# Kernel tuning notes

Measured on AMD Instinct MI355X. Metric: run time of the kernel, lower is better.

## Reference

```python
import jax, jax.numpy as jnp
import numpy as np

B, T, N, H, NHEADS, DFF, DEMO = 128, 128, 76, 64, 4, 256, 12

def _lin(x, W, b):
    # torch Linear: y = x @ W.T + b, W is [out, in]
    return jnp.matmul(x, W.T) + b

def _layernorm(x, g, b, eps=1e-7):
    mu = x.mean(-1, keepdims=True)
    var = ((x - mu) ** 2).mean(-1, keepdims=True)
    return (x - mu) / jnp.sqrt(var + eps) * g + b

def _gru_all_features(X, Wih, Whh, bih, bhh):
    # X: [B,T,N]; Wih: [N,3H] (input_size=1); Whh: [N,3H,H]; biases [N,3H]
    # PyTorch gate order: r, z, n. Returns H_seq [B,N,T,H].
    Bsz, Tlen, Nf = X.shape
    Hd = Whh.shape[-1]
    h0 = jnp.zeros((Bsz, Nf, Hd), X.dtype)
    def step(h, x_t):  # h [B,N,H], x_t [B,N]
        ih = x_t[:, :, None] * Wih[None] + bih[None]            # [B,N,3H]
        hh = jnp.einsum('bnh,ngh->bng', h, Whh) + bhh[None]     # [B,N,3H]
        r = jax.nn.sigmoid(ih[..., :Hd] + hh[..., :Hd])
        z = jax.nn.sigmoid(ih[..., Hd:2 * Hd] + hh[..., Hd:2 * Hd])
        n = jnp.tanh(ih[..., 2 * Hd:] + r * hh[..., 2 * Hd:])
        h_new = (1.0 - z) * n + z * h
        return h_new, h_new
    _, Hs = jax.lax.scan(step, h0, jnp.moveaxis(X, 1, 0))       # [T,B,N,H]
    return jnp.transpose(Hs, (1, 2, 0, 3))                      # [B,N,T,H]

def _time_attention(Hs, Wt, bt, Wx, bx, rate):
    # Hs [B,N,T,H]; Wt/Wx [N,H,H]; bt/bx [N,H]; rate [N]
    Tlen = Hs.shape[2]
    q = jnp.einsum('bnh,nkh->bnk', Hs[:, :, -1, :], Wt) + bt[None]          # [B,N,H]
    K = jnp.einsum('bnth,nkh->bntk', Hs, Wx) + bx[None, :, None, :]         # [B,N,T,H]
    dot = jnp.einsum('bnk,bntk->bnt', q, K)                                 # [B,N,T]
    tdecay = jnp.arange(1, Tlen + 1, dtype=Hs.dtype)                        # [1..T]
    ds = jax.nn.sigmoid(dot)
    denom = jax.nn.sigmoid(rate)[None, :, None] * jnp.log(2.72 + (1.0 - ds)) * tdecay
    denom = jnp.maximum(denom, 1e-6)
    e = jax.nn.relu(ds / denom)
    alpha = jax.nn.softmax(e, axis=-1)
    return jnp.einsum('bnt,bnth->bnh', alpha, Hs)                           # [B,N,H]

def _mha_decov(x, Wq, bq, Wk, bk, Wv, bv, Wo, bo, n_heads):
    Bsz, L, Dm = x.shape
    dk = Dm // n_heads
    def split(t):
        return t.reshape(Bsz, L, n_heads, dk).transpose(0, 2, 1, 3)
    q, k, v = split(_lin(x, Wq, bq)), split(_lin(x, Wk, bk)), split(_lin(x, Wv, bv))
    scores = jnp.matmul(q, k.transpose(0, 1, 3, 2)) / (dk ** 0.5)
    attn = jax.nn.softmax(scores, axis=-1)
    head = jnp.matmul(attn, v)                                              # [B,h,L,dk]
    merged = head.transpose(0, 2, 1, 3).reshape(Bsz, L, Dm)
    out = _lin(merged, Wo, bo)
    U = merged.reshape(Bsz * L, Dm)
    U = U - U.mean(0, keepdims=True)
    C = (U.T @ U) / max(Bsz * L, 1)
    decov = 0.5 * ((C ** 2).sum() - (jnp.diag(C) ** 2).sum())
    return out, decov

def setup_inputs():
    key = jax.random.key(0)
    ks = jax.random.split(key, 32)
    s = 0.08
    def rn(k, shape):
        return jax.random.normal(k, shape, jnp.float32) * s
    inp = {
        'X': jax.random.normal(ks[0], (B, T, N), jnp.float32),
        'D': jax.random.normal(ks[1], (B, DEMO), jnp.float32),
        'gru_Wih': rn(ks[2], (N, 3 * H)),
        'gru_Whh': rn(ks[3], (N, 3 * H, H)),
        'gru_bih': jnp.zeros((N, 3 * H), jnp.float32),
        'gru_bhh': jnp.zeros((N, 3 * H), jnp.float32),
        'att_Wt': rn(ks[4], (N, H, H)),
        'att_bt': jnp.zeros((N, H), jnp.float32),
        'att_Wx': rn(ks[5], (N, H, H)),
        'att_bx': jnp.zeros((N, H), jnp.float32),
        'att_rate': jnp.zeros((N,), jnp.float32),
        'demo_W': rn(ks[6], (H, DEMO)),
        'demo_b': jnp.zeros((H,), jnp.float32),
        'mh_Wq': rn(ks[7], (H, H)), 'mh_bq': rn(ks[8], (H,)),
        'mh_Wk': rn(ks[9], (H, H)), 'mh_bk': rn(ks[10], (H,)),
        'mh_Wv': rn(ks[11], (H, H)), 'mh_bv': rn(ks[12], (H,)),
        'mh_Wo': rn(ks[13], (H, H)), 'mh_bo': rn(ks[14], (H,)),
        'ln1_g': jnp.ones((H,), jnp.float32), 'ln1_b': jnp.zeros((H,), jnp.float32),
        'ffn_W1': rn(ks[15], (DFF, H)), 'ffn_b1': rn(ks[16], (DFF,)),
        'ffn_W2': rn(ks[17], (H, DFF)), 'ffn_b2': rn(ks[18], (H,)),
        'ln2_g': jnp.ones((H,), jnp.float32), 'ln2_b': jnp.zeros((H,), jnp.float32),
        'fa_Wq': rn(ks[19], (H, H)), 'fa_bq': rn(ks[20], (H,)),
        'fa_Wk': rn(ks[21], (H, H)), 'fa_bk': rn(ks[22], (H,)),
        'fa_Wv': rn(ks[23], (H, H)), 'fa_bv': rn(ks[24], (H,)),
        'fa_Wout': rn(ks[25], (1, H)), 'fa_bout': rn(ks[26], (1,)),
        'out0_W': rn(ks[27], (H, H)), 'out0_b': jnp.zeros((H,), jnp.float32),
        'out1_W': rn(ks[28], (1, H)), 'out1_b': jnp.zeros((1,), jnp.float32),
    }
    return inp

def _forward(X, D, gru_Wih, gru_Whh, gru_bih, gru_bhh, att_Wt, att_bt, att_Wx, att_bx,
             att_rate, demo_W, demo_b, mh_Wq, mh_bq, mh_Wk, mh_bk, mh_Wv, mh_bv, mh_Wo,
             mh_bo, ln1_g, ln1_b, ffn_W1, ffn_b1, ffn_W2, ffn_b2, ln2_g, ln2_b,
             fa_Wq, fa_bq, fa_Wk, fa_bk, fa_Wv, fa_bv, fa_Wout, fa_bout,
             out0_W, out0_b, out1_W, out1_b):
    Hs = _gru_all_features(X, gru_Wih, gru_Whh, gru_bih, gru_bhh)   # [B,N,T,H]
    F_dyn = _time_attention(Hs, att_Wt, att_bt, att_Wx, att_bx, att_rate)  # [B,N,H]
    f_demo = jnp.tanh(_lin(D, demo_W, demo_b))[:, None, :]
    F_in = jnp.concatenate([F_dyn, f_demo], axis=1)                 # [B,N+1,H]
    _, decov = _mha_decov(F_in, mh_Wq, mh_bq, mh_Wk, mh_bk, mh_Wv, mh_bv, mh_Wo, mh_bo, NHEADS)
    attn_out, _ = _mha_decov(_layernorm(F_in, ln1_g, ln1_b), mh_Wq, mh_bq, mh_Wk, mh_bk,
                             mh_Wv, mh_bv, mh_Wo, mh_bo, NHEADS)
    Y = F_in + attn_out
    z = _layernorm(Y, ln2_g, ln2_b)
    Z = Y + _lin(jax.nn.relu(_lin(z, ffn_W1, ffn_b1)), ffn_W2, ffn_b2)
    # FinalAttentionQKV
    Q = _lin(Z, fa_Wq, fa_bq)
    K = _lin(Z, fa_Wk, fa_bk)
    V = _lin(Z, fa_Wv, fa_bv)
    scores = _lin(Q * K, fa_Wout, fa_bout)[..., 0]                  # [B,L]
    alpha = jax.nn.softmax(scores, axis=1)
    s = jnp.einsum('bl,blh->bh', alpha, V)
    h = jax.nn.relu(_lin(s, out0_W, out0_b))
    y_prob = jax.nn.sigmoid(_lin(h, out1_W, out1_b))
    return y_prob, decov

def reference(X, D, gru_Wih, gru_Whh, gru_bih, gru_bhh, att_Wt, att_bt, att_Wx, att_bx,
              att_rate, demo_W, demo_b, mh_Wq, mh_bq, mh_Wk, mh_bk, mh_Wv, mh_bv, mh_Wo,
              mh_bo, ln1_g, ln1_b, ffn_W1, ffn_b1, ffn_W2, ffn_b2, ln2_g, ln2_b,
              fa_Wq, fa_bq, fa_Wk, fa_bk, fa_Wv, fa_bv, fa_Wout, fa_bout,
              out0_W, out0_b, out1_W, out1_b):
    return _forward(X, D, gru_Wih, gru_Whh, gru_bih, gru_bhh, att_Wt, att_bt, att_Wx,
                    att_bx, att_rate, demo_W, demo_b, mh_Wq, mh_bq, mh_Wk, mh_bk, mh_Wv,
                    mh_bv, mh_Wo, mh_bo, ln1_g, ln1_b, ffn_W1, ffn_b1, ffn_W2, ffn_b2,
                    ln2_g, ln2_b, fa_Wq, fa_bq, fa_Wk, fa_bk, fa_Wv, fa_bv, fa_Wout,
                    fa_bout, out0_W, out0_b, out1_W, out1_b)
```

## Files before the change

kernel.cpp:

```cpp
#include <hip/hip_runtime.h>
#include <math.h>

#define B_ 128
#define T_ 128
#define NF 76
#define HD 64
#define LQ 77

typedef __attribute__((ext_vector_type(8))) short short8v;
typedef __attribute__((ext_vector_type(4))) short short4v;
typedef __attribute__((ext_vector_type(4))) float f32x4;

__device__ __forceinline__ float frcp(float x) { return __builtin_amdgcn_rcpf(x); }
__device__ __forceinline__ float sigmf(float x) { return frcp(1.0f + __expf(-x)); }
__device__ __forceinline__ float sigm2(float x) { return frcp(1.0f + __builtin_amdgcn_exp2f(-x)); }
__device__ __forceinline__ float tanh_fast(float x) { return 2.0f * frcp(1.0f + __expf(-2.0f * x)) - 1.0f; }
__device__ __forceinline__ short tobf(float x) {
    unsigned u = __float_as_uint(x);
    u += 0x7FFF + ((u >> 16) & 1);
    return (short)(u >> 16);
}
__device__ __forceinline__ float bflo(unsigned u) { return __uint_as_float(u << 16); }
__device__ __forceinline__ float bfhi(unsigned u) { return __uint_as_float(u & 0xffff0000u); }

__global__ __launch_bounds__(256) void k_gru0(
    const float* __restrict__ X, const float* __restrict__ Wih,
    const float* __restrict__ Whh, const float* __restrict__ bih,
    const float* __restrict__ bhh,
    const float* __restrict__ Wt, const float* __restrict__ bt,
    const float* __restrict__ Wx, const float* __restrict__ bx,
    short* __restrict__ Hsg, float* __restrict__ qxg, float* __restrict__ qbg)
{
    __shared__ short As[8][16 * 68];
    __shared__ float xs[16 * 129];
    __shared__ float q1[16 * 65];
    __shared__ float q2[16 * 65];

    const int nf = blockIdx.y;
    const int chunk = blockIdx.x;
    const int cbase = chunk * 16;
    const int tid = threadIdx.x;
    const int w = tid >> 6;
    const int lane = tid & 63;
    const int col = lane & 15;
    const int quad = lane >> 4;

    const float S1 = 1.44269504f;
    const float S2 = 2.88539008f;

    for (int i = tid; i < 16 * T_; i += 256) {
        int b = i >> 7, t = i & 127;
        xs[b * 129 + t] = X[((size_t)(cbase + b) * T_ + t) * NF + nf];
    }

    short8v bfr[3][2];
    const float* wbase = Whh + (size_t)nf * 12288;
#pragma unroll
    for (int g3 = 0; g3 < 3; ++g3) {
        const float sc = (g3 == 2) ? S2 : S1;
#pragma unroll
        for (int k2 = 0; k2 < 2; ++k2) {
            int g = 64 * g3 + 16 * w + col;
            const float* src = wbase + g * 64 + 32 * k2 + quad * 8;
            float4 f0 = *(const float4*)src;
            float4 f1 = *(const float4*)(src + 4);
            short8v fr;
            fr[0] = tobf(f0.x * sc); fr[1] = tobf(f0.y * sc);
            fr[2] = tobf(f0.z * sc); fr[3] = tobf(f0.w * sc);
            fr[4] = tobf(f1.x * sc); fr[5] = tobf(f1.y * sc);
            fr[6] = tobf(f1.z * sc); fr[7] = tobf(f1.w * sc);
            bfr[g3][k2] = fr;
        }
    }

    const int c = 16 * w + col;
    const int base = nf * 192;
    const float wr = Wih[base + c] * S1;
    const float wz = Wih[base + 64 + c] * S1;
    const float wn = Wih[base + 128 + c] * S2;
    const float br = (bih[base + c] + bhh[base + c]) * S1;
    const float bz = (bih[base + 64 + c] + bhh[base + 64 + c]) * S1;
    const float bnn = bih[base + 128 + c] * S2;
    const float bhn = bhh[base + 128 + c] * S2;

    for (int i = tid; i < 16 * 68; i += 256) As[7][i] = 0;
    float hold[4];
#pragma unroll
    for (int r = 0; r < 4; ++r) hold[r] = 0.0f;
    __syncthreads();

    for (int t = 0; t < T_; ++t) {
        const int rb = (t + 7) & 7;
        const int wb = t & 7;
        const short* ap = &As[rb][col * 68 + quad * 8];
        short4v a0 = *(const short4v*)ap;
        short4v a1 = *(const short4v*)(ap + 4);
        short4v a2 = *(const short4v*)(ap + 32);
        short4v a3 = *(const short4v*)(ap + 36);
        short8v A0 = {a0[0], a0[1], a0[2], a0[3], a1[0], a1[1], a1[2], a1[3]};
        short8v A1 = {a2[0], a2[1], a2[2], a2[3], a3[0], a3[1], a3[2], a3[3]};

        f32x4 acc[3];
#pragma unroll
        for (int g3 = 0; g3 < 3; ++g3) {
            f32x4 a = {0.0f, 0.0f, 0.0f, 0.0f};
            a = __builtin_amdgcn_mfma_f32_16x16x32_bf16(A0, bfr[g3][0], a, 0, 0, 0);
            a = __builtin_amdgcn_mfma_f32_16x16x32_bf16(A1, bfr[g3][1], a, 0, 0, 0);
            acc[g3] = a;
        }

#pragma unroll
        for (int r = 0; r < 4; ++r) {
            float xv = xs[(quad * 4 + r) * 129 + t];
            float rr = sigm2(xv * wr + br + acc[0][r]);
            float zz = sigm2(xv * wz + bz + acc[1][r]);
            float nn = 2.0f * sigm2(xv * wn + bnn + rr * (acc[2][r] + bhn)) - 1.0f;
            hold[r] = nn + zz * (hold[r] - nn);
        }

#pragma unroll
        for (int r = 0; r < 4; ++r)
            As[wb][(quad * 4 + r) * 68 + c] = tobf(hold[r]);
        __syncthreads();

        if ((t & 7) == 7) {
            const int oct = tid & 7, bb = (tid >> 3) & 15, k0 = tid >> 7;
            short4v r0[4], r1[4];
#pragma unroll
            for (int s = 0; s < 4; ++s) {
                const short* p = &As[k0 + 2 * s][bb * 68 + oct * 8];
                r0[s] = *(const short4v*)p;
                r1[s] = *(const short4v*)(p + 4);
            }
            __syncthreads();
            const size_t gbase =
                (((size_t)nf * 128 + cbase + bb) * 128 + (t - 7)) * 64 + oct * 8;
#pragma unroll
            for (int s = 0; s < 4; ++s) {
                short8v v = {r0[s][0], r0[s][1], r0[s][2], r0[s][3],
                             r1[s][0], r1[s][1], r1[s][2], r1[s][3]};
                *(short8v*)(Hsg + gbase + (size_t)(k0 + 2 * s) * 64) = v;
            }
        }
    }

#pragma unroll
    for (int r = 0; r < 4; ++r)
        q1[(quad * 4 + r) * 65 + c] = hold[r];
    __syncthreads();
    for (int o = tid; o < 16 * 64; o += 256) {
        int b = o >> 6, k = o & 63;
        const float* wrow = Wt + ((size_t)nf * 64 + k) * 64;
        float a = bt[nf * 64 + k];
#pragma unroll 8
        for (int h = 0; h < 64; h += 4) {
            float4 wv = *(const float4*)&wrow[h];
            a += q1[b * 65 + h] * wv.x + q1[b * 65 + h + 1] * wv.y
               + q1[b * 65 + h + 2] * wv.z + q1[b * 65 + h + 3] * wv.w;
        }
        q2[b * 65 + k] = a;
    }
    __syncthreads();
    for (int o = tid; o < 16 * 64; o += 256) {
        int b = o >> 6, h = o & 63;
        float a = 0.0f;
#pragma unroll 8
        for (int k = 0; k < 64; ++k)
            a += q2[b * 65 + k] * Wx[((size_t)nf * 64 + k) * 64 + h];
        qxg[((size_t)nf * 128 + cbase + b) * 64 + h] = a;
    }
    for (int b = tid; b < 16; b += 256) {
        float a = 0.0f;
        for (int k = 0; k < 64; ++k) a += q2[b * 65 + k] * bx[nf * 64 + k];
        qbg[nf * 128 + cbase + b] = a;
    }
}

__global__ __launch_bounds__(128) void k_att(
    const short* __restrict__ Hsg, const float* __restrict__ qxg,
    const float* __restrict__ qbg, const float* __restrict__ rate,
    const float* __restrict__ D, const float* __restrict__ dW,
    const float* __restrict__ db, float* __restrict__ Sz,
    float* __restrict__ Fin)
{
    const int nf = blockIdx.x, b = blockIdx.y;
    const int tid = threadIdx.x;

    if (nf == NF) {
        if (tid < 64) {
            float acc = db[tid];
            for (int j = 0; j < 12; ++j) acc += D[b * 12 + j] * dW[tid * 12 + j];
            Fin[((size_t)b * LQ + 76) * HD + tid] = tanh_fast(acc);
        }
        int s0 = b * 33;
        for (int k = tid; k < 33; k += 128) {
            int idx = s0 + k;
            if (idx < 4161) Sz[idx] = 0.0f;
        }
        return;
    }

    __shared__ float wsum[128 * 69];
    __shared__ float wl[128];
    __shared__ float qxl[64];
    __shared__ float pn[2][68];
    __shared__ float pd[2];
    if (tid < 64) qxl[tid] = qxg[((size_t)nf * 128 + b) * 64 + tid];
    const float qb = qbg[nf * 128 + b];
    const float sigr = sigmf(rate[nf]);

    uint4 rv[8];
    const uint4* src = (const uint4*)(Hsg + (((size_t)nf * 128 + b) * 128 + tid) * 64);
#pragma unroll
    for (int k = 0; k < 8; ++k) rv[k] = src[k];
    __syncthreads();

    float a = qb;
#pragma unroll
    for (int k = 0; k < 8; ++k) {
        a += bflo(rv[k].x) * qxl[k * 8 + 0] + bfhi(rv[k].x) * qxl[k * 8 + 1]
           + bflo(rv[k].y) * qxl[k * 8 + 2] + bfhi(rv[k].y) * qxl[k * 8 + 3]
           + bflo(rv[k].z) * qxl[k * 8 + 4] + bfhi(rv[k].z) * qxl[k * 8 + 5]
           + bflo(rv[k].w) * qxl[k * 8 + 6] + bfhi(rv[k].w) * qxl[k * 8 + 7];
    }
    float ds = sigmf(a);
    float dn = fmaxf(sigr * __logf(2.72f + (1.0f - ds)) * (float)(tid + 1), 1e-6f);
    float e = fmaxf(ds * frcp(dn), 0.0f);
    float w = __expf(e);
    wl[tid] = w;
#pragma unroll
    for (int k = 0; k < 8; ++k) {
        float* d = &wsum[tid * 69 + k * 8];
        d[0] = w * bflo(rv[k].x); d[1] = w * bfhi(rv[k].x);
        d[2] = w * bflo(rv[k].y); d[3] = w * bfhi(rv[k].y);
        d[4] = w * bflo(rv[k].z); d[5] = w * bfhi(rv[k].z);
        d[6] = w * bflo(rv[k].w); d[7] = w * bfhi(rv[k].w);
    }
    __syncthreads();
    {
        int ch = tid & 63, half = tid >> 6;
        float acc = 0.0f, den = 0.0f;
        int t0 = half * 64;
        for (int t = t0; t < t0 + 64; ++t) {
            acc += wsum[t * 69 + ch];
            den += wl[t];
        }
        pn[half][ch] = acc;
        if (ch == 0) pd[half] = den;
    }
    __syncthreads();
    if (tid < 64) {
        float num = pn[0][tid] + pn[1][tid];
        float den = pd[0] + pd[1];
        Fin[((size_t)b * LQ + nf) * HD + tid] = num * frcp(den);
    }
}

__global__ __launch_bounds__(256) void k_mha2(
    const float* __restrict__ Fin,
    const float* __restrict__ Wq, const float* __restrict__ bq,
    const float* __restrict__ Wk, const float* __restrict__ bk,
    const float* __restrict__ Wv, const float* __restrict__ bv,
    const float* __restrict__ g1, const float* __restrict__ b1,
    float* __restrict__ M1, float* __restrict__ M2)
{
    __shared__ float xl[LQ * 68];
    __shared__ float qh[LQ * 20], kh[LQ * 20], vh[LQ * 20];
    float (*os)[17] = (float (*)[17])xl;
    const int b = blockIdx.x, hd = blockIdx.y, v = blockIdx.z;
    const int tid = threadIdx.x;
    const float* xsrc = Fin + (size_t)b * LQ * HD;

    for (int idx = tid; idx < LQ * HD; idx += 256)
        xl[(idx >> 6) * 68 + (idx & 63)] = xsrc[idx];
    __syncthreads();
    if (v == 1) {
        if (tid < LQ) {
            float mu = 0.0f;
            for (int h = 0; h < 64; ++h) mu += xl[tid * 68 + h];
            mu *= (1.0f / 64.0f);
            float var = 0.0f;
            for (int h = 0; h < 64; ++h) { float d = xl[tid * 68 + h] - mu; var += d * d; }
            var *= (1.0f / 64.0f);
            float rs = rsqrtf(var + 1e-7f);
            for (int h = 0; h < 64; ++h)
                xl[tid * 68 + h] = (xl[tid * 68 + h] - mu) * rs * g1[h] + b1[h];
        }
        __syncthreads();
    }

    for (int idx = tid; idx < LQ * 16; idx += 256) {
        int l = idx >> 4, d = idx & 15, ch = hd * 16 + d;
        float aq = bq[ch], ak = bk[ch], av = bv[ch];
        const float4* wq = (const float4*)(Wq + ch * 64);
        const float4* wk = (const float4*)(Wk + ch * 64);
        const float4* wv = (const float4*)(Wv + ch * 64);
        const float4* xr = (const float4*)&xl[l * 68];
#pragma unroll 4
        for (int c4 = 0; c4 < 16; ++c4) {
            float4 xv = xr[c4];
            float4 a = wq[c4], bb = wk[c4], cc = wv[c4];
            aq += xv.x * a.x + xv.y * a.y + xv.z * a.z + xv.w * a.w;
            ak += xv.x * bb.x + xv.y * bb.y + xv.z * bb.z + xv.w * bb.w;
            av += xv.x * cc.x + xv.y * cc.y + xv.z * cc.z + xv.w * cc.w;
        }
        qh[l * 20 + d] = aq; kh[l * 20 + d] = ak; vh[l * 20 + d] = av;
    }
    __syncthreads();

    if (tid < 231) {
        int l = tid % 77, third = tid / 77;
        float4 qf0 = *(const float4*)&qh[l * 20 + 0];
        float4 qf1 = *(const float4*)&qh[l * 20 + 4];
        float4 qf2 = *(const float4*)&qh[l * 20 + 8];
        float4 qf3 = *(const float4*)&qh[l * 20 + 12];
        int j0 = third * 26;
        int j1 = (third == 2) ? LQ : j0 + 26;
        float o[16];
#pragma unroll
        for (int d = 0; d < 16; ++d) o[d] = 0.0f;
        float ss = 0.0f;
        for (int j = j0; j < j1; ++j) {
            const float4* kp = (const float4*)&kh[j * 20];
            float4 k0 = kp[0], k1 = kp[1], k2 = kp[2], k3 = kp[3];
            float sc = qf0.x * k0.x + qf0.y * k0.y + qf0.z * k0.z + qf0.w * k0.w
                     + qf1.x * k1.x + qf1.y * k1.y + qf1.z * k1.z + qf1.w * k1.w
                     + qf2.x * k2.x + qf2.y * k2.y + qf2.z * k2.z + qf2.w * k2.w
                     + qf3.x * k3.x + qf3.y * k3.y + qf3.z * k3.z + qf3.w * k3.w;
            float p = __expf(sc * 0.25f);
            ss += p;
            const float4* vp = (const float4*)&vh[j * 20];
            float4 v0 = vp[0], v1 = vp[1], v2 = vp[2], v3 = vp[3];
            o[0] += p * v0.x; o[1] += p * v0.y; o[2] += p * v0.z; o[3] += p * v0.w;
            o[4] += p * v1.x; o[5] += p * v1.y; o[6] += p * v1.z; o[7] += p * v1.w;
            o[8] += p * v2.x; o[9] += p * v2.y; o[10] += p * v2.z; o[11] += p * v2.w;
            o[12] += p * v3.x; o[13] += p * v3.y; o[14] += p * v3.z; o[15] += p * v3.w;
        }
#pragma unroll
        for (int d = 0; d < 16; ++d) os[tid][d] = o[d];
        os[tid][16] = ss;
    }
    __syncthreads();
    if (tid < LQ) {
        float inv = frcp(os[tid][16] + os[77 + tid][16] + os[154 + tid][16]);
        float* Mout = (v == 1) ? M2 : M1;
#pragma unroll
        for (int d = 0; d < 16; ++d)
            Mout[((size_t)b * LQ + tid) * HD + hd * 16 + d]
                = (os[tid][d] + os[77 + tid][d] + os[154 + tid][d]) * inv;
    }
}

__global__ __launch_bounds__(256) void k_zff(
    const float* __restrict__ Fin, float* __restrict__ M2,
    const float* __restrict__ Wo, const float* __restrict__ bo,
    const float* __restrict__ g2, const float* __restrict__ b2,
    const float* __restrict__ W1, const float* __restrict__ bb1,
    const float* __restrict__ W2, const float* __restrict__ bb2,
    const float* __restrict__ faWq, const float* __restrict__ fabq,
    const float* __restrict__ faWk, const float* __restrict__ fabk,
    const float* __restrict__ faWv, const float* __restrict__ fabv,
    const float* __restrict__ faWout, const float* __restrict__ fabout,
    float* __restrict__ scout)
{
    __shared__ float m2l[16 * 68];
    __shared__ float yl[16 * 68];
    __shared__ float zl[16 * 68];
    __shared__ float ul[16 * 260];
    const int tid = threadIdx.x;
    const size_t base = (size_t)blockIdx.x * 16;
    const size_t eb = base * 64;
    const int h = tid & 63, rq = tid >> 6;

    for (int idx = tid; idx < 1024; idx += 256)
        m2l[(idx >> 6) * 68 + (idx & 63)] = M2[eb + idx];
    __syncthreads();

    {
        float acc[4];
#pragma unroll
        for (int rr = 0; rr < 4; ++rr) acc[rr] = bo[h];
        const float4* wo = (const float4*)(Wo + h * 64);
#pragma unroll 4
        for (int c4 = 0; c4 < 16; ++c4) {
            float4 wv = wo[c4];
#pragma unroll
            for (int rr = 0; rr < 4; ++rr) {
                float4 mv = *(const float4*)&m2l[(rq * 4 + rr) * 68 + c4 * 4];
                acc[rr] += mv.x * wv.x + mv.y * wv.y + mv.z * wv.z + mv.w * wv.w;
            }
        }
#pragma unroll
        for (int rr = 0; rr < 4; ++rr) {
            int r = rq * 4 + rr;
            yl[r * 68 + h] = Fin[eb + r * 64 + h] + acc[rr];
        }
    }
    __syncthreads();
    if (tid < 16) {
        float mu = 0.0f;
        for (int c = 0; c < 64; ++c) mu += yl[tid * 68 + c];
        mu *= (1.0f / 64.0f);
        float var = 0.0f;
        for (int c = 0; c < 64; ++c) { float d = yl[tid * 68 + c] - mu; var += d * d; }
        var *= (1.0f / 64.0f);
        float rs = rsqrtf(var + 1e-7f);
        for (int c = 0; c < 64; ++c)
            zl[tid * 68 + c] = (yl[tid * 68 + c] - mu) * rs * g2[c] + b2[c];
    }
    __syncthreads();

    {
        const int f = tid;
        float acc[16];
#pragma unroll
        for (int r = 0; r < 16; ++r) acc[r] = bb1[f];
        const float4* w1r = (const float4*)(W1 + f * 64);
#pragma unroll
        for (int c = 0; c < 4; ++c) {
            float4 w0 = w1r[c * 4 + 0], w1 = w1r[c * 4 + 1];
            float4 w2 = w1r[c * 4 + 2], w3 = w1r[c * 4 + 3];
#pragma unroll
            for (int r = 0; r < 16; ++r) {
                const float4* zr = (const float4*)&zl[r * 68 + c * 16];
                float4 z0 = zr[0], z1 = zr[1], z2 = zr[2], z3 = zr[3];
                acc[r] += z0.x * w0.x + z0.y * w0.y + z0.z * w0.z + z0.w * w0.w
                        + z1.x * w1.x + z1.y * w1.y + z1.z * w1.z + z1.w * w1.w
                        + z2.x * w2.x + z2.y * w2.y + z2.z * w2.z + z2.w * w2.w
                        + z3.x * w3.x + z3.y * w3.y + z3.z * w3.z + z3.w * w3.w;
            }
        }
#pragma unroll
        for (int r = 0; r < 16; ++r) ul[r * 260 + f] = fmaxf(acc[r], 0.0f);
    }
    __syncthreads();
    {
        float acc[4];
#pragma unroll
        for (int rr = 0; rr < 4; ++rr) acc[rr] = bb2[h];
        const float4* w2r = (const float4*)(W2 + h * 256);
#pragma unroll 4
        for (int c = 0; c < 16; ++c) {
            float4 w0 = w2r[c * 4 + 0], w1 = w2r[c * 4 + 1];
            float4 w2 = w2r[c * 4 + 2], w3 = w2r[c * 4 + 3];
#pragma unroll
            for (int rr = 0; rr < 4; ++rr) {
                const float4* ur = (const float4*)&ul[(rq * 4 + rr) * 260 + c * 16];
                float4 u0 = ur[0], u1 = ur[1], u2 = ur[2], u3 = ur[3];
                acc[rr] += u0.x * w0.x + u0.y * w0.y + u0.z * w0.z + u0.w * w0.w
                         + u1.x * w1.x + u1.y * w1.y + u1.z * w1.z + u1.w * w1.w
                         + u2.x * w2.x + u2.y * w2.y + u2.z * w2.z + u2.w * w2.w
                         + u3.x * w3.x + u3.y * w3.y + u3.z * w3.z + u3.w * w3.w;
            }
        }
#pragma unroll
        for (int rr = 0; rr < 4; ++rr)
            yl[(rq * 4 + rr) * 68 + h] += acc[rr];
    }
    __syncthreads();

    {
        const float4* wq = (const float4*)(faWq + h * 64);
        const float4* wk = (const float4*)(faWk + h * 64);
        const float4* wv = (const float4*)(faWv + h * 64);
        float q[4], k[4], v[4];
#pragma unroll
        for (int rr = 0; rr < 4; ++rr) { q[rr] = fabq[h]; k[rr] = fabk[h]; v[rr] = fabv[h]; }
#pragma unroll 4
        for (int c4 = 0; c4 < 16; ++c4) {
            float4 a = wq[c4], bb = wk[c4], cc = wv[c4];
#pragma unroll
            for (int rr = 0; rr < 4; ++rr) {
                float4 zv = *(const float4*)&yl[(rq * 4 + rr) * 68 + c4 * 4];
                q[rr] += zv.x * a.x + zv.y * a.y + zv.z * a.z + zv.w * a.w;
                k[rr] += zv.x * bb.x + zv.y * bb.y + zv.z * bb.z + zv.w * bb.w;
                v[rr] += zv.x * cc.x + zv.y * cc.y + zv.z * cc.z + zv.w * cc.w;
            }
        }
        float fw = faWout[h];
#pragma unroll
        for (int rr = 0; rr < 4; ++rr) {
            int r = rq * 4 + rr;
            ul[r * 68 + h] = q[rr] * k[rr] * fw;
            M2[eb + r * 64 + h] = v[rr];
        }
    }
    __syncthreads();
    if (tid < 16) {
        float a = fabout[0];
        for (int c = 0; c < 64; ++c) a += ul[tid * 68 + c];
        scout[base + tid] = a;
    }
}

__global__ __launch_bounds__(256) void k_cov(
    const float* __restrict__ M1, float* __restrict__ S, float* __restrict__ MU,
    unsigned* __restrict__ cnt, float* __restrict__ out)
{
    __shared__ float tile[64 * 64];
    const int tid = threadIdx.x;
    const int ig = tid >> 6, j = tid & 63;
    const int i = blockIdx.x * 4 + ig;
    const int l0 = blockIdx.y * 308;
    float acc = 0.0f, mua = 0.0f;
    for (int c0 = 0; c0 < 308; c0 += 64) {
        int rows = (308 - c0 < 64) ? (308 - c0) : 64;
        __syncthreads();
        const float4* gsrc = (const float4*)(M1 + (size_t)(l0 + c0) * 64);
        for (int idx = tid; idx < rows * 16; idx += 256)
            *(float4*)&tile[idx * 4] = gsrc[idx];
        __syncthreads();
#pragma unroll 4
        for (int l = 0; l < rows; ++l) {
            float v = tile[l * 64 + j];
            acc += tile[l * 64 + i] * v;
            mua += v;
        }
    }
    atomicAdd(&S[i * 64 + j], acc);
    if (blockIdx.x == 0 && ig == 0) atomicAdd(&MU[j], mua);
    __threadfence();
    __syncthreads();
    __shared__ unsigned lastf;
    if (tid == 0) lastf = (atomicAdd(cnt, 1u) == 511u);
    __syncthreads();
    if (lastf) {
        __shared__ float mus[64];
        __shared__ float pa[4], pd[4];
        if (tid < 64) mus[tid] = atomicAdd(&MU[tid], 0.0f);
        __syncthreads();
        const float invM = 1.0f / 9856.0f;
        float asum = 0.0f, dsum = 0.0f;
        for (int idx = tid; idx < 4096; idx += 256) {
            int ii = idx >> 6, jj = idx & 63;
            float c = atomicAdd(&S[idx], 0.0f) * invM - (mus[ii] * invM) * (mus[jj] * invM);
            asum += c * c;
            if (ii == jj) dsum += c * c;
        }
        for (int o = 32; o; o >>= 1) {
            asum += __shfl_xor(asum, o, 64);
            dsum += __shfl_xor(dsum, o, 64);
        }
        if ((tid & 63) == 0) { pa[tid >> 6] = asum; pd[tid >> 6] = dsum; }
        __syncthreads();
        if (tid == 0)
            out[128] = 0.5f * ((pa[0] + pa[1] + pa[2] + pa[3])
                             - (pd[0] + pd[1] + pd[2] + pd[3]));
    }
}

__global__ __launch_bounds__(128) void k_head(
    const float* __restrict__ Vg, const float* __restrict__ scout,
    const float* __restrict__ o0W, const float* __restrict__ o0b,
    const float* __restrict__ o1W, const float* __restrict__ o1b,
    float* __restrict__ out)
{
    __shared__ float sl[LQ + 3];
    __shared__ float pn[2][64];
    __shared__ float sv[64], h1[64];
    __shared__ float red0;
    const int b = blockIdx.x, tid = threadIdx.x;

    if (tid < LQ) sl[tid] = scout[b * LQ + tid];
    __syncthreads();
    if (tid < 64) {
        float v0 = sl[tid];
        float v1 = (tid < LQ - 64) ? sl[tid + 64] : -1e30f;
        float m = fmaxf(v0, v1);
        for (int o = 32; o; o >>= 1) m = fmaxf(m, __shfl_xor(m, o, 64));
        float e0 = __expf(v0 - m);
        float e1 = (tid < LQ - 64) ? __expf(v1 - m) : 0.0f;
        float s = e0 + e1;
        for (int o = 32; o; o >>= 1) s += __shfl_xor(s, o, 64);
        sl[tid] = e0;
        if (tid < LQ - 64) sl[tid + 64] = e1;
        if (tid == 0) red0 = s;
    }
    __syncthreads();
    {
        int h = tid & 63, half = tid >> 6;
        int l0 = half ? 39 : 0, l1 = half ? LQ : 39;
        float acc = 0.0f;
#pragma unroll 4
        for (int l = l0; l < l1; ++l)
            acc += sl[l] * Vg[((size_t)b * LQ + l) * 64 + h];
        pn[half][h] = acc;
    }
    __syncthreads();
    if (tid < 64) sv[tid] = (pn[0][tid] + pn[1][tid]) * frcp(red0);
    __syncthreads();
    if (tid < 64) {
        float acc = o0b[tid];
        const float4* w = (const float4*)(o0W + tid * 64);
#pragma unroll 4
        for (int c4 = 0; c4 < 16; ++c4) {
            float4 wv = w[c4];
            const float4* sp = (const float4*)&sv[c4 * 4];
            float4 s0 = sp[0];
            acc += s0.x * wv.x + s0.y * wv.y + s0.z * wv.z + s0.w * wv.w;
        }
        h1[tid] = fmaxf(acc, 0.0f);
    }
    __syncthreads();
    if (tid < 64) {
        float p = h1[tid] * o1W[tid];
        for (int o = 32; o; o >>= 1) p += __shfl_xor(p, o, 64);
        if (tid == 0) out[b] = sigmf(p + o1b[0]);
    }
}

__global__ void k_demo(const float* __restrict__ D, const float* __restrict__ dW,
                       const float* __restrict__ db, float* __restrict__ Fin)
{
    int b = blockIdx.x, h = threadIdx.x;
    float acc = db[h];
    for (int j = 0; j < 12; ++j) acc += D[b * 12 + j] * dW[h * 12 + j];
    Fin[((size_t)b * LQ + 76) * HD + h] = tanh_fast(acc);
}

__global__ void k_zero(float* __restrict__ p)
{
    for (int i = threadIdx.x; i < 4161; i += 256) p[i] = 0.0f;
}

__global__ __launch_bounds__(128) void k_gru_mfma(
    const float* __restrict__ X, const float* __restrict__ Wih,
    const float* __restrict__ Whh, const float* __restrict__ bih,
    const float* __restrict__ bhh,
    const float* __restrict__ Wt, const float* __restrict__ bt,
    const float* __restrict__ Wx, const float* __restrict__ bx,
    const float* __restrict__ rate, float* __restrict__ Fin)
{
    __shared__ short As[2][16 * 68];
    __shared__ float xs[16 * 129];
    __shared__ float q1[16 * 65];
    __shared__ float q2[16 * 65];
    __shared__ float qbs[16];
    __shared__ float dotw[2][2][16];

    const int nf = blockIdx.y;
    const int cbase = blockIdx.x * 16;
    const int tid = threadIdx.x;
    const int w = tid >> 6;
    const int lane = tid & 63;
    const int col = lane & 15;
    const int quad = lane >> 4;

    for (int i = tid; i < 16 * T_; i += 128) {
        int b = i >> 7, t = i & 127;
        xs[b * 129 + t] = X[((size_t)(cbase + b) * T_ + t) * NF + nf];
    }
    short8v bfr[3][2][2];
    const float* wbase = Whh + (size_t)nf * 12288;
#pragma unroll
    for (int g3 = 0; g3 < 3; ++g3)
#pragma unroll
        for (int s = 0; s < 2; ++s)
#pragma unroll
            for (int k2 = 0; k2 < 2; ++k2) {
                int g = 64 * g3 + 32 * w + 16 * s + col;
                const float* src = wbase + g * 64 + 32 * k2 + quad * 8;
                float4 f0 = *(const float4*)src;
                float4 f1 = *(const float4*)(src + 4);
                short8v fr;
                fr[0] = tobf(f0.x); fr[1] = tobf(f0.y); fr[2] = tobf(f0.z); fr[3] = tobf(f0.w);
                fr[4] = tobf(f1.x); fr[5] = tobf(f1.y); fr[6] = tobf(f1.z); fr[7] = tobf(f1.w);
                bfr[g3][s][k2] = fr;
            }
    float wr[2], wz[2], wn[2], br[2], bz[2], bnn[2], bhn[2];
#pragma unroll
    for (int s = 0; s < 2; ++s) {
        int c = 32 * w + 16 * s + col;
        int base = nf * 192;
        wr[s] = Wih[base + c]; wz[s] = Wih[base + 64 + c]; wn[s] = Wih[base + 128 + c];
        br[s] = bih[base + c] + bhh[base + c];
        bz[s] = bih[base + 64 + c] + bhh[base + 64 + c];
        bnn[s] = bih[base + 128 + c]; bhn[s] = bhh[base + 128 + c];
    }
    const float sigr = sigmf(rate[nf]);
    float hold[2][4], num[2][4], den[4], qxv[2][4], qbv[4];
#pragma unroll
    for (int r = 0; r < 4; ++r) {
        den[r] = 0.0f; qbv[r] = 0.0f;
        num[0][r] = 0.0f; num[1][r] = 0.0f;
        qxv[0][r] = 0.0f; qxv[1][r] = 0.0f;
    }
    for (int pass = 0; pass < 2; ++pass) {
        for (int i = tid; i < 16 * 68; i += 128) As[0][i] = 0;
#pragma unroll
        for (int s = 0; s < 2; ++s)
#pragma unroll
            for (int r = 0; r < 4; ++r) hold[s][r] = 0.0f;
        __syncthreads();
        for (int t = 0; t < T_; ++t) {
            const int rb = t & 1;
            const int wb = 1 - rb;
            const short* ap = &As[rb][col * 68 + quad * 8];
            short4v a0 = *(const short4v*)ap;
            short4v a1 = *(const short4v*)(ap + 4);
            short4v a2 = *(const short4v*)(ap + 32);
            short4v a3 = *(const short4v*)(ap + 36);
            short8v A0 = {a0[0], a0[1], a0[2], a0[3], a1[0], a1[1], a1[2], a1[3]};
            short8v A1 = {a2[0], a2[1], a2[2], a2[3], a3[0], a3[1], a3[2], a3[3]};
            f32x4 acc[3][2];
#pragma unroll
            for (int g3 = 0; g3 < 3; ++g3)
#pragma unroll
                for (int s = 0; s < 2; ++s) {
                    f32x4 a = {0.0f, 0.0f, 0.0f, 0.0f};
                    a = __builtin_amdgcn_mfma_f32_16x16x32_bf16(A0, bfr[g3][s][0], a, 0, 0, 0);
                    a = __builtin_amdgcn_mfma_f32_16x16x32_bf16(A1, bfr[g3][s][1], a, 0, 0, 0);
                    acc[g3][s] = a;
                }
            float xv[4];
#pragma unroll
            for (int r = 0; r < 4; ++r) xv[r] = xs[(quad * 4 + r) * 129 + t];
            float hnew[2][4];
#pragma unroll
            for (int s = 0; s < 2; ++s)
#pragma unroll
                for (int r = 0; r < 4; ++r) {
                    float rr = sigmf(xv[r] * wr[s] + br[s] + acc[0][s][r]);
                    float zz = sigmf(xv[r] * wz[s] + bz[s] + acc[1][s][r]);
                    float nn = tanh_fast(xv[r] * wn[s] + bnn[s] + rr * (acc[2][s][r] + bhn[s]));
                    hnew[s][r] = (1.0f - zz) * nn + zz * hold[s][r];
                    hold[s][r] = hnew[s][r];
                }
#pragma unroll
            for (int s = 0; s < 2; ++s)
#pragma unroll
                for (int r = 0; r < 4; ++r)
                    As[wb][(quad * 4 + r) * 68 + 32 * w + 16 * s + col] = tobf(hnew[s][r]);
            if (pass == 1) {
                float p[4];
#pragma unroll
                for (int r = 0; r < 4; ++r)
                    p[r] = qxv[0][r] * hnew[0][r] + qxv[1][r] * hnew[1][r];
#pragma unroll
                for (int m = 1; m < 16; m <<= 1) {
                    p[0] += __shfl_xor(p[0], m, 64);
                    p[1] += __shfl_xor(p[1], m, 64);
                    p[2] += __shfl_xor(p[2], m, 64);
                    p[3] += __shfl_xor(p[3], m, 64);
                }
                if (col == 0) {
#pragma unroll
                    for (int r = 0; r < 4; ++r) dotw[rb][w][quad * 4 + r] = p[r];
                }
                __syncthreads();
                float tf = (float)(t + 1);
#pragma unroll
                for (int r = 0; r < 4; ++r) {
                    float dot = p[r] + dotw[rb][1 - w][quad * 4 + r] + qbv[r];
                    float ds = sigmf(dot);
                    float dn = fmaxf(sigr * __logf(2.72f + (1.0f - ds)) * tf, 1e-6f);
                    float e = fmaxf(ds * frcp(dn), 0.0f);
                    float wt = __expf(e);
                    den[r] += wt;
                    num[0][r] += wt * hnew[0][r];
                    num[1][r] += wt * hnew[1][r];
                }
            } else {
                __syncthreads();
            }
        }
        if (pass == 0) {
#pragma unroll
            for (int s = 0; s < 2; ++s)
#pragma unroll
                for (int r = 0; r < 4; ++r)
                    q1[(quad * 4 + r) * 65 + 32 * w + 16 * s + col] = hold[s][r];
            __syncthreads();
            for (int o = tid; o < 16 * 64; o += 128) {
                int b = o >> 6, k = o & 63;
                const float* wrow = Wt + ((size_t)nf * 64 + k) * 64;
                float a = bt[nf * 64 + k];
#pragma unroll 8
                for (int h = 0; h < 64; h += 4) {
                    float4 wv = *(const float4*)&wrow[h];
                    a += q1[b * 65 + h] * wv.x + q1[b * 65 + h + 1] * wv.y
                       + q1[b * 65 + h + 2] * wv.z + q1[b * 65 + h + 3] * wv.w;
                }
                q2[b * 65 + k] = a;
            }
            __syncthreads();
            for (int o = tid; o < 16 * 64; o += 128) {
                int b = o >> 6, h = o & 63;
                float a = 0.0f;
#pragma unroll 8
                for (int k = 0; k < 64; ++k)
                    a += q2[b * 65 + k] * Wx[((size_t)nf * 64 + k) * 64 + h];
                q1[b * 65 + h] = a;
            }
            for (int b = tid; b < 16; b += 128) {
                float a = 0.0f;
                for (int k = 0; k < 64; ++k) a += q2[b * 65 + k] * bx[nf * 64 + k];
                qbs[b] = a;
            }
            __syncthreads();
#pragma unroll
            for (int r = 0; r < 4; ++r) {
                qbv[r] = qbs[quad * 4 + r];
#pragma unroll
                for (int s = 0; s < 2; ++s)
                    qxv[s][r] = q1[(quad * 4 + r) * 65 + 32 * w + 16 * s + col];
                den[r] = 0.0f; num[0][r] = 0.0f; num[1][r] = 0.0f;
            }
            __syncthreads();
        }
    }
#pragma unroll
    for (int s = 0; s < 2; ++s)
#pragma unroll
        for (int r = 0; r < 4; ++r) {
            int b = cbase + quad * 4 + r;
            int c = 32 * w + 16 * s + col;
            Fin[((size_t)b * LQ + nf) * HD + c] = num[s][r] * frcp(den[r]);
        }
}

extern "C" void kernel_launch(void* const* d_in, const int* in_sizes, int n_in,
                              void* d_out, int out_size, void* d_ws, size_t ws_size,
                              hipStream_t stream)
{
    (void)in_sizes; (void)n_in; (void)out_size;
    const float* X     = (const float*)d_in[0];
    const float* D     = (const float*)d_in[1];
    const float* gWih  = (const float*)d_in[2];
    const float* gWhh  = (const float*)d_in[3];
    const float* gbih  = (const float*)d_in[4];
    const float* gbhh  = (const float*)d_in[5];
    const float* aWt   = (const float*)d_in[6];
    const float* abt   = (const float*)d_in[7];
    const float* aWx   = (const float*)d_in[8];
    const float* abx   = (const float*)d_in[9];
    const float* arate = (const float*)d_in[10];
    const float* dW    = (const float*)d_in[11];
    const float* db    = (const float*)d_in[12];
    const float* mWq   = (const float*)d_in[13]; const float* mbq = (const float*)d_in[14];
    const float* mWk   = (const float*)d_in[15]; const float* mbk = (const float*)d_in[16];
    const float* mWv   = (const float*)d_in[17]; const float* mbv = (const float*)d_in[18];
    const float* mWo   = (const float*)d_in[19]; const float* mbo = (const float*)d_in[20];
    const float* l1g   = (const float*)d_in[21]; const float* l1b = (const float*)d_in[22];
    const float* fW1   = (const float*)d_in[23]; const float* fb1 = (const float*)d_in[24];
    const float* fW2   = (const float*)d_in[25]; const float* fb2 = (const float*)d_in[26];
    const float* l2g   = (const float*)d_in[27]; const float* l2b = (const float*)d_in[28];
    const float* faWq  = (const float*)d_in[29]; const float* fabq = (const float*)d_in[30];
    const float* faWk  = (const float*)d_in[31]; const float* fabk = (const float*)d_in[32];
    const float* faWv  = (const float*)d_in[33]; const float* fabv = (const float*)d_in[34];
    const float* faWo  = (const float*)d_in[35]; const float* fabo = (const float*)d_in[36];
    const float* o0W   = (const float*)d_in[37]; const float* o0b  = (const float*)d_in[38];
    const float* o1W   = (const float*)d_in[39]; const float* o1b  = (const float*)d_in[40];

    float* ws  = (float*)d_ws;
    float* Fin = ws;
    float* M1  = Fin + 630784;
    float* M2  = M1  + 630784;
    float* S   = M2  + 630784;
    float* MU  = S   + 4096;
    unsigned* cnt = (unsigned*)(MU + 64);
    float* qxg = MU + 128;
    float* scout = qxg + 622592;
    short* Hsg = (short*)(scout + 9856);
    const size_t need = (size_t)(630784 * 3 + 4096 + 128 + 622592 + 9856) * 4
                        + (size_t)79691776 * 2;
    float* outp = (float*)d_out;
    float* qbg = scout;

    if (ws_size >= need) {
        k_gru0<<<dim3(8, NF), 256, 0, stream>>>(X, gWih, gWhh, gbih, gbhh,
                                                aWt, abt, aWx, abx, Hsg, qxg, qbg);
        k_att<<<dim3(NF + 1, B_), 128, 0, stream>>>(Hsg, qxg, qbg, arate,
                                                    D, dW, db, S, Fin);
    } else {
        k_gru_mfma<<<dim3(8, NF), 128, 0, stream>>>(X, gWih, gWhh, gbih, gbhh,
                                                    aWt, abt, aWx, abx, arate, Fin);
        k_demo<<<B_, 64, 0, stream>>>(D, dW, db, Fin);
        k_zero<<<1, 256, 0, stream>>>(S);
    }
    k_mha2<<<dim3(B_, 4, 2), 256, 0, stream>>>(Fin, mWq, mbq, mWk, mbk, mWv, mbv,
                                               l1g, l1b, M1, M2);
    k_zff<<<616, 256, 0, stream>>>(Fin, M2, mWo, mbo, l2g, l2b,
                                   fW1, fb1, fW2, fb2,
                                   faWq, fabq, faWk, fabk, faWv, fabv,
                                   faWo, fabo, scout);
    k_cov<<<dim3(16, 32), 256, 0, stream>>>(M1, S, MU, cnt, outp);
    k_head<<<B_, 128, 0, stream>>>(M2, scout, o0W, o0b, o1W, o1b, outp);
}
```

Measured before the change: 519.6 us.

## Fold covariance into FFN kernel, parallelize layernorm, seed GRU MFMA with biases

The covariance-reduction kernel becomes extra blocks appended to the FFN/attention kernel's grid, which removes one launch and lets both workloads run concurrently. The second layernorm inside that kernel now spreads each row over 16 lanes with shuffle reductions instead of 16 serial threads. It also switches to a single-pass E[x²]−μ² variance, which can lose some precision. In the GRU recurrence the gate biases seed the MFMA accumulators, the gate math uses fmaf, and setprio is raised around the MFMA block to shorten the per-step dependent chain.

```diff
diff --git a/kernel.cpp b/kernel.cpp
--- a/kernel.cpp
+++ b/kernel.cpp
@@ -78,10 +78,16 @@
     const float wr = Wih[base + c] * S1;
     const float wz = Wih[base + 64 + c] * S1;
     const float wn = Wih[base + 128 + c] * S2;
-    const float br = (bih[base + c] + bhh[base + c]) * S1;
-    const float bz = (bih[base + 64 + c] + bhh[base + 64 + c]) * S1;
     const float bnn = bih[base + 128 + c] * S2;
-    const float bhn = bhh[base + 128 + c] * S2;
+    f32x4 biasC[3];
+    {
+        float brr = (bih[base + c] + bhh[base + c]) * S1;
+        float bzz = (bih[base + 64 + c] + bhh[base + 64 + c]) * S1;
+        float bhn = bhh[base + 128 + c] * S2;
+        biasC[0] = (f32x4){brr, brr, brr, brr};
+        biasC[1] = (f32x4){bzz, bzz, bzz, bzz};
+        biasC[2] = (f32x4){bhn, bhn, bhn, bhn};
+    }
 
     for (int i = tid; i < 16 * 68; i += 256) As[7][i] = 0;
     float hold[4];
@@ -100,22 +106,25 @@
         short8v A0 = {a0[0], a0[1], a0[2], a0[3], a1[0], a1[1], a1[2], a1[3]};
         short8v A1 = {a2[0], a2[1], a2[2], a2[3], a3[0], a3[1], a3[2], a3[3]};
 
+        __builtin_amdgcn_s_setprio(1);
         f32x4 acc[3];
 #pragma unroll
         for (int g3 = 0; g3 < 3; ++g3) {
-            f32x4 a = {0.0f, 0.0f, 0.0f, 0.0f};
-            a = __builtin_amdgcn_mfma_f32_16x16x32_bf16(A0, bfr[g3][0], a, 0, 0, 0);
-            a = __builtin_amdgcn_mfma_f32_16x16x32_bf16(A1, bfr[g3][1], a, 0, 0, 0);
-            acc[g3] = a;
-        }
+            f32x4 a = __builtin_amdgcn_mfma_f32_16x16x32_bf16(
+                A0, bfr[g3][0], biasC[g3], 0, 0, 0);
+            acc[g3] = __builtin_amdgcn_mfma_f32_16x16x32_bf16(
+                A1, bfr[g3][1], a, 0, 0, 0);
+        }
+        __builtin_amdgcn_s_setprio(0);
 
 #pragma unroll
         for (int r = 0; r < 4; ++r) {
             float xv = xs[(quad * 4 + r) * 129 + t];
-            float rr = sigm2(xv * wr + br + acc[0][r]);
-            float zz = sigm2(xv * wz + bz + acc[1][r]);
-            float nn = 2.0f * sigm2(xv * wn + bnn + rr * (acc[2][r] + bhn)) - 1.0f;
-            hold[r] = nn + zz * (hold[r] - nn);
+            float rr = sigm2(fmaf(xv, wr, acc[0][r]));
+            float zz = sigm2(fmaf(xv, wz, acc[1][r]));
+            float uu = sigm2(fmaf(rr, acc[2][r], fmaf(xv, wn, bnn)));
+            float nn = fmaf(2.0f, uu, -1.0f);
+            hold[r] = fmaf(zz, hold[r] - nn, nn);
         }
 
 #pragma unroll
@@ -361,13 +370,73 @@
     const float* __restrict__ faWk, const float* __restrict__ fabk,
     const float* __restrict__ faWv, const float* __restrict__ fabv,
     const float* __restrict__ faWout, const float* __restrict__ fabout,
-    float* __restrict__ scout)
+    float* __restrict__ scout,
+    const float* __restrict__ M1, float* __restrict__ S,
+    float* __restrict__ MU, unsigned* __restrict__ cnt,
+    float* __restrict__ covout)
 {
     __shared__ float m2l[16 * 68];
     __shared__ float yl[16 * 68];
     __shared__ float zl[16 * 68];
     __shared__ float ul[16 * 260];
+    __shared__ unsigned lastf;
+    __shared__ float mus[64];
+    __shared__ float pa[4], pd[4];
     const int tid = threadIdx.x;
+
+    if (blockIdx.x >= 616) {
+        float* tile = ul;
+        const int cid = blockIdx.x - 616;
+        const int bxc = cid & 15, byc = cid >> 4;
+        const int ig = tid >> 6, j = tid & 63;
+        const int i = bxc * 4 + ig;
+        const int l0 = byc * 308;
+        float acc = 0.0f, mua = 0.0f;
+        for (int c0 = 0; c0 < 308; c0 += 64) {
+            int rows = (308 - c0 < 64) ? (308 - c0) : 64;
+            __syncthreads();
+            const float4* gsrc = (const float4*)(M1 + (size_t)(l0 + c0) * 64);
+            for (int idx = tid; idx < rows * 16; idx += 256)
+                *(float4*)&tile[idx * 4] = gsrc[idx];
+            __syncthreads();
+#pragma unroll 4
+            for (int l = 0; l < rows; ++l) {
+                float v = tile[l * 64 + j];
+                acc += tile[l * 64 + i] * v;
+                mua += v;
+            }
+        }
+        atomicAdd(&S[i * 64 + j], acc);
+        if (bxc == 0 && ig == 0) atomicAdd(&MU[j], mua);
+        __threadfence();
+        __syncthreads();
+        if (tid == 0) lastf = (atomicAdd(cnt, 1u) == 511u);
+        __syncthreads();
+        if (lastf) {
+            if (tid < 64) mus[tid] = atomicAdd(&MU[tid], 0.0f);
+            __syncthreads();
+            const float invM = 1.0f / 9856.0f;
+            float asum = 0.0f, dsum = 0.0f;
+            for (int idx = tid; idx < 4096; idx += 256) {
+                int ii = idx >> 6, jj = idx & 63;
+                float cc = atomicAdd(&S[idx], 0.0f) * invM
+                         - (mus[ii] * invM) * (mus[jj] * invM);
+                asum += cc * cc;
+                if (ii == jj) dsum += cc * cc;
+            }
+            for (int o = 32; o; o >>= 1) {
+                asum += __shfl_xor(asum, o, 64);
+                dsum += __shfl_xor(dsum, o, 64);
+            }
+            if ((tid & 63) == 0) { pa[tid >> 6] = asum; pd[tid >> 6] = dsum; }
+            __syncthreads();
+            if (tid == 0)
+                covout[128] = 0.5f * ((pa[0] + pa[1] + pa[2] + pa[3])
+                                    - (pd[0] + pd[1] + pd[2] + pd[3]));
+        }
+        return;
+    }
+
     const size_t base = (size_t)blockIdx.x * 16;
     const size_t eb = base * 64;
     const int h = tid & 63, rq = tid >> 6;
@@ -397,16 +466,25 @@
         }
     }
     __syncthreads();
-    if (tid < 16) {
-        float mu = 0.0f;
-        for (int c = 0; c < 64; ++c) mu += yl[tid * 68 + c];
-        mu *= (1.0f / 64.0f);
-        float var = 0.0f;
-        for (int c = 0; c < 64; ++c) { float d = yl[tid * 68 + c] - mu; var += d * d; }
-        var *= (1.0f / 64.0f);
+    {
+        int row = tid >> 4, l16 = tid & 15;
+        float s = 0.0f, s2 = 0.0f;
+#pragma unroll
+        for (int c = l16; c < 64; c += 16) {
+            float vv = yl[row * 68 + c];
+            s += vv; s2 += vv * vv;
+        }
+#pragma unroll
+        for (int m = 1; m < 16; m <<= 1) {
+            s += __shfl_xor(s, m);
+            s2 += __shfl_xor(s2, m);
+        }
+        float mu = s * (1.0f / 64.0f);
+        float var = s2 * (1.0f / 64.0f) - mu * mu;
         float rs = rsqrtf(var + 1e-7f);
-        for (int c = 0; c < 64; ++c)
-            zl[tid * 68 + c] = (yl[tid * 68 + c] - mu) * rs * g2[c] + b2[c];
+#pragma unroll
+        for (int c = l16; c < 64; c += 16)
+            zl[row * 68 + c] = (yl[row * 68 + c] - mu) * rs * g2[c] + b2[c];
     }
     __syncthreads();
 
@@ -490,62 +568,6 @@
         float a = fabout[0];
         for (int c = 0; c < 64; ++c) a += ul[tid * 68 + c];
         scout[base + tid] = a;
-    }
-}
-
-__global__ __launch_bounds__(256) void k_cov(
-    const float* __restrict__ M1, float* __restrict__ S, float* __restrict__ MU,
-    unsigned* __restrict__ cnt, float* __restrict__ out)
-{
-    __shared__ float tile[64 * 64];
-    const int tid = threadIdx.x;
-    const int ig = tid >> 6, j = tid & 63;
-    const int i = blockIdx.x * 4 + ig;
-    const int l0 = blockIdx.y * 308;
-    float acc = 0.0f, mua = 0.0f;
-    for (int c0 = 0; c0 < 308; c0 += 64) {
-        int rows = (308 - c0 < 64) ? (308 - c0) : 64;
-        __syncthreads();
-        const float4* gsrc = (const float4*)(M1 + (size_t)(l0 + c0) * 64);
-        for (int idx = tid; idx < rows * 16; idx += 256)
-            *(float4*)&tile[idx * 4] = gsrc[idx];
-        __syncthreads();
-#pragma unroll 4
-        for (int l = 0; l < rows; ++l) {
-            float v = tile[l * 64 + j];
-            acc += tile[l * 64 + i] * v;
-            mua += v;
-        }
-    }
-    atomicAdd(&S[i * 64 + j], acc);
-    if (blockIdx.x == 0 && ig == 0) atomicAdd(&MU[j], mua);
-    __threadfence();
-    __syncthreads();
-    __shared__ unsigned lastf;
-    if (tid == 0) lastf = (atomicAdd(cnt, 1u) == 511u);
-    __syncthreads();
-    if (lastf) {
-        __shared__ float mus[64];
-        __shared__ float pa[4], pd[4];
-        if (tid < 64) mus[tid] = atomicAdd(&MU[tid], 0.0f);
-        __syncthreads();
-        const float invM = 1.0f / 9856.0f;
-        float asum = 0.0f, dsum = 0.0f;
-        for (int idx = tid; idx < 4096; idx += 256) {
-            int ii = idx >> 6, jj = idx & 63;
-            float c = atomicAdd(&S[idx], 0.0f) * invM - (mus[ii] * invM) * (mus[jj] * invM);
-            asum += c * c;
-            if (ii == jj) dsum += c * c;
-        }
-        for (int o = 32; o; o >>= 1) {
-            asum += __shfl_xor(asum, o, 64);
-            dsum += __shfl_xor(dsum, o, 64);
-        }
-        if ((tid & 63) == 0) { pa[tid >> 6] = asum; pd[tid >> 6] = dsum; }
-        __syncthreads();
-        if (tid == 0)
-            out[128] = 0.5f * ((pa[0] + pa[1] + pa[2] + pa[3])
-                             - (pd[0] + pd[1] + pd[2] + pd[3]));
     }
 }
 
@@ -880,10 +902,10 @@
     }
     k_mha2<<<dim3(B_, 4, 2), 256, 0, stream>>>(Fin, mWq, mbq, mWk, mbk, mWv, mbv,
                                                l1g, l1b, M1, M2);
-    k_zff<<<616, 256, 0, stream>>>(Fin, M2, mWo, mbo, l2g, l2b,
-                                   fW1, fb1, fW2, fb2,
-                                   faWq, fabq, faWk, fabk, faWv, fabv,
-                                   faWo, fabo, scout);
-    k_cov<<<dim3(16, 32), 256, 0, stream>>>(M1, S, MU, cnt, outp);
+    k_zff<<<1128, 256, 0, stream>>>(Fin, M2, mWo, mbo, l2g, l2b,
+                                    fW1, fb1, fW2, fb2,
+                                    faWq, fabq, faWk, fabk, faWv, fabv,
+                                    faWo, fabo, scout,
+                                    M1, S, MU, cnt, outp);
     k_head<<<B_, 128, 0, stream>>>(M2, scout, o0W, o0b, o1W, o1b, outp);
 }
```

Result: faster. 492.1 us (-5.3%).
